# Performance work log

Measured on AMD Instinct MI355X. Metric: run time of the kernel, lower is better.

The kernel has to match this reference:

```python
import jax, jax.numpy as jnp
import numpy as np

N = 100000
E = 3200000
IN_C, HID_C, OUT_C = 128, 128, 64


def setup_inputs() -> dict:
    key = jax.random.key(0)
    k_x, k_e, k_w1, k_w2 = jax.random.split(key, 4)
    x = jax.random.normal(k_x, (N, IN_C), dtype=jnp.float32)
    edge_index = jax.random.randint(k_e, (2, E), 0, N, dtype=jnp.int64)
    # GCNConv uses Glorot-init weight [in, out] and zero bias
    W1 = jax.random.normal(k_w1, (IN_C, HID_C), dtype=jnp.float32) * (1.0 / np.sqrt(IN_C))
    b1 = jnp.zeros((HID_C,), dtype=jnp.float32)
    W2 = jax.random.normal(k_w2, (HID_C, OUT_C), dtype=jnp.float32) * (1.0 / np.sqrt(HID_C))
    b2 = jnp.zeros((OUT_C,), dtype=jnp.float32)
    return {"x": x, "edge_index": edge_index, "W1": W1, "b1": b1, "W2": W2, "b2": b2}


def _gcn_norm(edge_index, n_nodes):
    """Add self-loops and compute symmetric normalization coefficients."""
    loop = jnp.arange(n_nodes, dtype=edge_index.dtype)
    src = jnp.concatenate([edge_index[0], loop])  # [E+N]
    dst = jnp.concatenate([edge_index[1], loop])  # [E+N]
    ones = jnp.ones(src.shape[0], dtype=jnp.float32)
    deg = jax.ops.segment_sum(ones, dst, num_segments=n_nodes)  # in-degree w/ self loops
    dinv = jnp.where(deg > 0, jax.lax.rsqrt(deg), 0.0)
    norm = dinv[src] * dinv[dst]  # [E+N]
    return src, dst, norm


def _gcn_conv(x, W, b, src, dst, norm, n_nodes):
    h = x @ W                                   # [N, out] dense transform first (PyG order)
    msg = norm[:, None] * h[src]                # gather + scale  [E+N, out]
    out = jax.ops.segment_sum(msg, dst, num_segments=n_nodes)  # scatter-add
    return out + b


def reference(x, edge_index, W1, b1, W2, b2):
    src, dst, norm = _gcn_norm(edge_index, N)
    h = _gcn_conv(x, W1, b1, src, dst, norm, N)
    h = jax.nn.relu(h)
    out = _gcn_conv(h, W2, b2, src, dst, norm, N)
    return out
```

## Files before the change

### kernel.cpp

```cpp
#include <hip/hip_runtime.h>

typedef unsigned int u32;
typedef unsigned short u16;
typedef unsigned long long u64;
typedef __bf16 bf16x8 __attribute__((ext_vector_type(8)));
typedef float floatx4 __attribute__((ext_vector_type(4)));
typedef float floatx2 __attribute__((ext_vector_type(2)));
typedef u32 u32x2 __attribute__((ext_vector_type(2)));
typedef u32 u32x4 __attribute__((ext_vector_type(4)));


__device__ __forceinline__ u16 f2bf(float f) {
  u32 u = __float_as_uint(f);
  u += 0x7fffu + ((u >> 16) & 1u);
  return (u16)(u >> 16);
}
__device__ __forceinline__ float bflo(u32 v) { return __uint_as_float(v << 16); }
__device__ __forceinline__ float bfhi(u32 v) { return __uint_as_float(v & 0xffff0000u); }
__device__ __forceinline__ floatx2 bf2(u32 v) {
  floatx2 r; r.x = bflo(v); r.y = bfhi(v); return r;
}

#define SLICE_SH 10
#define SL (1 << SLICE_SH)
#define MAXNS 128
#define NBBIN 320
#define BTH 512
#define SRC_BITS 17

__device__ __forceinline__ void gemm1_body(const float* __restrict__ X,
                                           const float* __restrict__ W,
                                           u16* __restrict__ Y, int nrows,
                                           int bid, u16* Wt) {
  constexpr int K = 128, OUT = 128, NT = 8, LDW = 136;
  int tid = threadIdx.x;
  for (int idx = tid; idx < K * OUT; idx += BTH) {
    int k = idx >> 7, n = idx & 127;
    Wt[n * LDW + k] = f2bf(W[idx]);
  }
  __syncthreads();
  int lane = tid & 63, wave = tid >> 6;
  int quad = lane >> 4, low = lane & 15;
  int mBase = bid * 128 + wave * 16;
  int m = mBase + low;
  int ml = (m < nrows) ? m : (nrows - 1);
  floatx4 acc[NT];
#pragma unroll
  for (int i = 0; i < NT; i++) acc[i] = (floatx4)0.0f;
#pragma unroll
  for (int kb = 0; kb < 4; kb++) {
    int k0 = kb * 32 + quad * 8;
    floatx4 p0 = *(const floatx4*)(X + (size_t)ml * K + k0);
    floatx4 p1 = *(const floatx4*)(X + (size_t)ml * K + k0 + 4);
    union { bf16x8 v; u16 s[8]; } au;
#pragma unroll
    for (int j = 0; j < 4; j++) { au.s[j] = f2bf(p0[j]); au.s[4 + j] = f2bf(p1[j]); }
#pragma unroll
    for (int nt = 0; nt < NT; nt++) {
      bf16x8 b = *(const bf16x8*)(&Wt[(nt * 16 + low) * LDW + k0]);
      acc[nt] = __builtin_amdgcn_mfma_f32_16x16x32_bf16(au.v, b, acc[nt], 0, 0, 0);
    }
  }
#pragma unroll
  for (int nt = 0; nt < NT; nt++) {
    int col = nt * 16 + low;
#pragma unroll
    for (int r = 0; r < 4; r++) {
      int row = mBase + quad * 4 + r;
      if (row < nrows) Y[(size_t)row * OUT + col] = f2bf(acc[nt][r]);
    }
  }
}

__device__ __forceinline__ void bin_body(const int* __restrict__ ei,
                                         int* __restrict__ scur,
                                         u32* __restrict__ stA, u32* __restrict__ stB,
                                         int splitS, int cap, int e, int ns,
                                         int bid, int* hist, int* curs) {
  int per = (e + NBBIN - 1) / NBBIN;
  int e0 = bid * per;
  int e1 = e0 + per; if (e1 > e) e1 = e;
  for (int t = threadIdx.x; t < ns; t += BTH) hist[t] = 0;
  __syncthreads();
  for (int i = e0 + threadIdx.x; i < e1; i += BTH) {
    int d = ei[e + i];
    atomicAdd(&hist[d >> SLICE_SH], 1);
  }
  __syncthreads();
  for (int t = threadIdx.x; t < ns; t += BTH)
    curs[t] = atomicAdd(&scur[t], hist[t]);
  __syncthreads();
  int i = e0 + threadIdx.x;
  for (; i + 3 * BTH < e1; i += 4 * BTH) {
    int d[4], s[4], pos[4];
#pragma unroll
    for (int p = 0; p < 4; p++) {
      int ii = i + BTH * p;
      s[p] = ei[ii]; d[p] = ei[e + ii];
    }
#pragma unroll
    for (int p = 0; p < 4; p++) pos[p] = atomicAdd(&curs[d[p] >> SLICE_SH], 1);
#pragma unroll
    for (int p = 0; p < 4; p++) {
      int sl = d[p] >> SLICE_SH;
      u32* st = (sl < splitS) ? stA + (size_t)sl * cap : stB + (size_t)(sl - splitS) * cap;
      st[pos[p]] = ((u32)(d[p] & (SL - 1)) << SRC_BITS) | (u32)s[p];
    }
  }
  for (; i < e1; i += BTH) {
    int s = ei[i], d = ei[e + i];
    int sl = d >> SLICE_SH;
    u32* st = (sl < splitS) ? stA + (size_t)sl * cap : stB + (size_t)(sl - splitS) * cap;
    st[atomicAdd(&curs[sl], 1)] = ((u32)(d & (SL - 1)) << SRC_BITS) | (u32)s;
  }
}

__global__ __launch_bounds__(BTH) void gemm1_bin(const float* __restrict__ X,
                                                 const float* __restrict__ W1,
                                                 u16* __restrict__ Y, int nrows, int nbGemm,
                                                 const int* __restrict__ ei,
                                                 int* __restrict__ scur,
                                                 u32* __restrict__ stA, u32* __restrict__ stB,
                                                 int splitS, int cap, int e, int ns) {
  __shared__ __attribute__((aligned(16))) char smbuf[128 * 136 * 2];
  int id = blockIdx.x;
  int small = (NBBIN < nbGemm) ? NBBIN : nbGemm;
  int isBin, bid;
  if (id < 2 * small) { isBin = !(id & 1); bid = id >> 1; }
  else { bid = small + (id - 2 * small); isBin = (NBBIN > nbGemm); }
  if (isBin) {
    int* hist = (int*)smbuf;
    int* curs = hist + MAXNS;
    bin_body(ei, scur, stA, stB, splitS, cap, e, ns, bid, hist, curs);
  } else {
    gemm1_body(X, W1, Y, nrows, bid, (u16*)smbuf);
  }
}

__global__ __launch_bounds__(1024) void fill_slice3(const u32* __restrict__ stA,
                                                    const u32* __restrict__ stB,
                                                    const int* __restrict__ scur,
                                                    int* __restrict__ rp,
                                                    float* __restrict__ dinv,
                                                    int* __restrict__ csr,
                                                    int splitS, int cap, int n, int ns) {
  __shared__ int cnt[SL];
  __shared__ int part[SL];
  __shared__ int sb[MAXNS];
  const int s = blockIdx.x;
  const int base = s << SLICE_SH;
  const int tid = threadIdx.x;
  cnt[tid] = 0;
  if (tid < MAXNS) sb[tid] = (tid < ns) ? scur[tid] : 0;
  __syncthreads();
  for (int off = 1; off < MAXNS; off <<= 1) {
    int v = 0;
    if (tid < MAXNS && tid >= off) v = sb[tid - off];
    __syncthreads();
    if (tid < MAXNS) sb[tid] += v;
    __syncthreads();
  }
  const int csrLo = s ? sb[s - 1] : 0;
  const int m = sb[s] - csrLo;
  if (s == ns - 1 && tid == 0) rp[n] = sb[ns - 1];
  const u32* st = (s < splitS) ? stA + (size_t)s * cap : stB + (size_t)(s - splitS) * cap;
  {
    int i = tid;
    for (; i + 7168 < m; i += 8192) {
      int b[8];
#pragma unroll
      for (int p = 0; p < 8; p++) b[p] = (int)(st[i + 1024 * p] >> SRC_BITS);
#pragma unroll
      for (int p = 0; p < 8; p++) atomicAdd(&cnt[b[p]], 1);
    }
    for (; i < m; i += 1024)
      atomicAdd(&cnt[(int)(st[i] >> SRC_BITS)], 1);
  }
  __syncthreads();
  int c0 = cnt[tid];
  part[tid] = c0;
  __syncthreads();
  for (int off = 1; off < SL; off <<= 1) {
    int t = (tid >= off) ? part[tid - off] : 0;
    __syncthreads();
    part[tid] += t;
    __syncthreads();
  }
  int p0 = csrLo + (tid ? part[tid - 1] : 0);
  __syncthreads();
  cnt[tid] = p0;
  int d0 = base + tid;
  if (d0 < n) { rp[d0] = p0; dinv[d0] = rsqrtf((float)(c0 + 1)); }
  __syncthreads();
  {
    int i = tid;
    for (; i + 7168 < m; i += 8192) {
      u32 pr[8]; int pos[8];
#pragma unroll
      for (int p = 0; p < 8; p++) pr[p] = st[i + 1024 * p];
#pragma unroll
      for (int p = 0; p < 8; p++)
        pos[p] = atomicAdd(&cnt[pr[p] >> SRC_BITS], 1);
#pragma unroll
      for (int p = 0; p < 8; p++) csr[pos[p]] = (int)(pr[p] & ((1u << SRC_BITS) - 1u));
    }
    for (; i < m; i += 1024) {
      u32 pr = st[i];
      int pos = atomicAdd(&cnt[pr >> SRC_BITS], 1);
      csr[pos] = (int)(pr & ((1u << SRC_BITS) - 1u));
    }
  }
}

__global__ __launch_bounds__(256) void agg128_g2(const u32* __restrict__ H,
                                                 const int* __restrict__ rp,
                                                 const int* __restrict__ cs,
                                                 const float* __restrict__ dinv,
                                                 const float* __restrict__ b1,
                                                 const float* __restrict__ W2,
                                                 u16* __restrict__ h2, int n) {
  __shared__ u16 Wt[64 * 136];
  __shared__ u16 Arow[16 * 136];
  const int tid = threadIdx.x;
  for (int idx = tid; idx < 128 * 64; idx += 256) {
    int k = idx >> 6, nn = idx & 63;
    Wt[nn * 136 + k] = f2bf(W2[idx]);
  }
  const int nodeBase = blockIdx.x * 4;
  const int wave = tid >> 6, lane = tid & 63;
  int node = nodeBase + wave;
  int nodeC = (node < n) ? node : (n - 1);
  int e4 = lane >> 4, c = lane & 15;
  int s0 = rp[nodeC], s1 = rp[nodeC + 1];
  floatx2 a2[4];
#pragma unroll
  for (int k = 0; k < 4; k++) a2[k] = (floatx2)0.0f;
  for (int base = s0; base < s1; base += 64) {
    int nb = s1 - base; if (nb > 64) nb = 64;
    int src = 0; float dv = 0.f;
    if (lane < nb) { src = cs[base + lane]; dv = dinv[src]; }
    for (int j = 0; j < nb; j += 16) {
      u32x4 v[4]; float w[4];
#pragma unroll
      for (int p = 0; p < 4; p++) {
        int idx = j + 4 * p + e4;
        int sj = __shfl(src, idx);
        w[p] = __shfl(dv, idx);
        v[p] = *(const u32x4*)(H + (size_t)sj * 64 + 4 * c);
      }
#pragma unroll
      for (int p = 0; p < 4; p++) {
        floatx2 wp; wp.x = w[p]; wp.y = w[p];
#pragma unroll
        for (int k = 0; k < 4; k++) {
          a2[k] += wp * bf2(v[p][k]);
        }
      }
    }
  }
#pragma unroll
  for (int k = 0; k < 4; k++) {
    a2[k].x += __shfl_xor(a2[k].x, 16);
    a2[k].y += __shfl_xor(a2[k].y, 16);
    a2[k].x += __shfl_xor(a2[k].x, 32);
    a2[k].y += __shfl_xor(a2[k].y, 32);
  }
  float ds = dinv[nodeC];
  u32x4 vs = *(const u32x4*)(H + (size_t)nodeC * 64 + 4 * c);
  floatx4 bb0 = *(const floatx4*)(b1 + 8 * c);
  floatx4 bb1 = *(const floatx4*)(b1 + 8 * c + 4);
  float r[8];
#pragma unroll
  for (int k = 0; k < 4; k++) {
    r[2 * k]     = ds * (a2[k].x + ds * bflo(vs[k]));
    r[2 * k + 1] = ds * (a2[k].y + ds * bfhi(vs[k]));
  }
#pragma unroll
  for (int k = 0; k < 4; k++) { r[k] += bb0[k]; r[4 + k] += bb1[k]; }
#pragma unroll
  for (int k = 0; k < 8; k++) r[k] = fmaxf(r[k], 0.f);
  if (e4 == 0) {
    union { u16 s[8]; u32x4 v; } pk;
#pragma unroll
    for (int k = 0; k < 8; k++) pk.s[k] = f2bf(r[k]);
    *(u32x4*)&Arow[wave * 136 + 8 * c] = pk.v;
  }
  __syncthreads();
  const int quad = e4, low = c;
  floatx4 acc = (floatx4)0.0f;
#pragma unroll
  for (int kb = 0; kb < 4; kb++) {
    int k0 = kb * 32 + quad * 8;
    bf16x8 af = *(const bf16x8*)&Arow[low * 136 + k0];
    bf16x8 bf = *(const bf16x8*)&Wt[(wave * 16 + low) * 136 + k0];
    acc = __builtin_amdgcn_mfma_f32_16x16x32_bf16(af, bf, acc, 0, 0, 0);
  }
  if (quad == 0) {
#pragma unroll
    for (int rI = 0; rI < 4; rI++) {
      int row = nodeBase + rI;
      if (row < n) h2[(size_t)row * 64 + wave * 16 + low] = f2bf(acc[rI]);
    }
  }
}

__global__ __launch_bounds__(256) void agg_64(const u16* __restrict__ Hu,
                                              const int* __restrict__ rp,
                                              const int* __restrict__ cs,
                                              const float* __restrict__ dinv,
                                              const float* __restrict__ b2,
                                              float* __restrict__ out, int n) {
  const u32* H = (const u32*)Hu;
  int node = blockIdx.x * 4 + (threadIdx.x >> 6);
  if (node >= n) return;
  int lane = threadIdx.x & 63;
  int e4 = lane >> 4, c = lane & 15;
  int s0 = rp[node], s1 = rp[node + 1];
  floatx2 a2[2];
  a2[0] = (floatx2)0.0f; a2[1] = (floatx2)0.0f;
  for (int base = s0; base < s1; base += 64) {
    int nb = s1 - base; if (nb > 64) nb = 64;
    int src = 0; float dv = 0.f;
    if (lane < nb) { src = cs[base + lane]; dv = dinv[src]; }
    for (int j = 0; j < nb; j += 16) {
      u32x2 v[4]; float w[4];
#pragma unroll
      for (int p = 0; p < 4; p++) {
        int idx = j + 4 * p + e4;
        int sj = __shfl(src, idx);
        w[p] = __shfl(dv, idx);
        v[p] = *(const u32x2*)(H + (size_t)sj * 32 + 2 * c);
      }
#pragma unroll
      for (int p = 0; p < 4; p++) {
        floatx2 wp; wp.x = w[p]; wp.y = w[p];
        a2[0] += wp * bf2(v[p].x);
        a2[1] += wp * bf2(v[p].y);
      }
    }
  }
#pragma unroll
  for (int k = 0; k < 2; k++) {
    a2[k].x += __shfl_xor(a2[k].x, 16);
    a2[k].y += __shfl_xor(a2[k].y, 16);
    a2[k].x += __shfl_xor(a2[k].x, 32);
    a2[k].y += __shfl_xor(a2[k].y, 32);
  }
  float ds = dinv[node];
  u32x2 vs = *(const u32x2*)(H + (size_t)node * 32 + 2 * c);
  floatx4 bf = *(const floatx4*)(b2 + 4 * c);
  if (e4 == 0) {
    floatx4 o;
    o[0] = ds * (a2[0].x + ds * bflo(vs.x)) + bf[0];
    o[1] = ds * (a2[0].y + ds * bfhi(vs.x)) + bf[1];
    o[2] = ds * (a2[1].x + ds * bflo(vs.y)) + bf[2];
    o[3] = ds * (a2[1].y + ds * bfhi(vs.y)) + bf[3];
    *(floatx4*)(out + (size_t)node * 64 + 4 * c) = o;
  }
}


extern "C" void kernel_launch(void* const* d_in, const int* in_sizes, int n_in,
                              void* d_out, int out_size, void* d_ws, size_t ws_size,
                              hipStream_t stream) {
  const float* x  = (const float*)d_in[0];
  const int*   ei = (const int*)d_in[1];
  const float* W1 = (const float*)d_in[2];
  const float* b1 = (const float*)d_in[3];
  const float* W2 = (const float*)d_in[4];
  const float* b2 = (const float*)d_in[5];
  const int N = in_sizes[0] / 128;
  const int E = in_sizes[1] / 2;
  const int NS = (N + SL - 1) >> SLICE_SH;

  int CAP = (E + NS - 1) / NS;
  CAP += CAP / 8;
  size_t doutSlots = (size_t)out_size / 4;
  int SPLIT = (int)(doutSlots / (size_t)CAP);
  if (SPLIT > NS) SPLIT = NS;

  auto al = [](size_t v) { return (v + 255) & ~(size_t)255; };
  char* ws = (char*)d_ws;
  size_t o = 0;
  int*   scur  = (int*)(ws + o);  o += 512;
  int*   rp    = (int*)(ws + o);  o += al((size_t)(N + 1) * 4);
  float* dinv  = (float*)(ws + o); o += al((size_t)N * 4);
  int*   csr   = (int*)(ws + o);  o += al((size_t)E * 4);
  u16*   h     = (u16*)(ws + o);  o += al((size_t)N * 128 * 2);
  u16*   h2    = (u16*)(ws + o);  o += al((size_t)N * 128 * 2);
  u32* stA = (u32*)d_out;
  u32* stB = (u32*)h2;

  const int nbGemm = (N + 127) / 128;

  hipMemsetAsync(scur, 0, 512, stream);
  gemm1_bin<<<NBBIN + nbGemm, BTH, 0, stream>>>(x, W1, h, N, nbGemm,
                                                ei, scur, stA, stB, SPLIT, CAP, E, NS);
  fill_slice3<<<NS, 1024, 0, stream>>>(stA, stB, scur, rp, dinv, csr, SPLIT, CAP, N, NS);
  agg128_g2<<<(N + 3) / 4, 256, 0, stream>>>((const u32*)h, rp, csr, dinv, b1, W2, h2, N);
  agg_64<<<(N + 3) / 4, 256, 0, stream>>>(h2, rp, csr, dinv, b2, (float*)d_out, N);
}
```

Before: 368.8 us.

## Halve CSR slice size and stage slice edges in LDS for counting sort

Node slices shrink from 1024 to 512 nodes, so there are twice as many slices and the edges of each slice (about 16k) fit in shared memory. The fill kernel copies the slice's packed edges into LDS once, then runs both the histogram pass and the scatter pass from LDS instead of reading global memory twice. The binning kernel gets half as many bin blocks. The risks are that the shared staging array (about 120KB) limits occupancy to one block per CU, and there is no check that a slice's edge count fits in CAPMAX.

```diff
diff --git a/kernel.cpp b/kernel.cpp
--- a/kernel.cpp
+++ b/kernel.cpp
@@ -21,12 +21,13 @@
   floatx2 r; r.x = bflo(v); r.y = bfhi(v); return r;
 }
 
-#define SLICE_SH 10
+#define SLICE_SH 9
 #define SL (1 << SLICE_SH)
-#define MAXNS 128
-#define NBBIN 320
+#define MAXNS 256
+#define NBBIN 160
 #define BTH 512
 #define SRC_BITS 17
+#define CAPMAX 30000
 
 __device__ __forceinline__ void gemm1_body(const float* __restrict__ X,
                                            const float* __restrict__ W,
@@ -137,20 +138,21 @@
   }
 }
 
-__global__ __launch_bounds__(1024) void fill_slice3(const u32* __restrict__ stA,
+__global__ __launch_bounds__(1024) void fill_slice5(const u32* __restrict__ stA,
                                                     const u32* __restrict__ stB,
                                                     const int* __restrict__ scur,
                                                     int* __restrict__ rp,
                                                     float* __restrict__ dinv,
                                                     int* __restrict__ csr,
                                                     int splitS, int cap, int n, int ns) {
+  __shared__ u32 stg[CAPMAX];
   __shared__ int cnt[SL];
   __shared__ int part[SL];
   __shared__ int sb[MAXNS];
   const int s = blockIdx.x;
   const int base = s << SLICE_SH;
   const int tid = threadIdx.x;
-  cnt[tid] = 0;
+  if (tid < SL) cnt[tid] = 0;
   if (tid < MAXNS) sb[tid] = (tid < ns) ? scur[tid] : 0;
   __syncthreads();
   for (int off = 1; off < MAXNS; off <<= 1) {
@@ -164,51 +166,31 @@
   const int m = sb[s] - csrLo;
   if (s == ns - 1 && tid == 0) rp[n] = sb[ns - 1];
   const u32* st = (s < splitS) ? stA + (size_t)s * cap : stB + (size_t)(s - splitS) * cap;
-  {
-    int i = tid;
-    for (; i + 7168 < m; i += 8192) {
-      int b[8];
-#pragma unroll
-      for (int p = 0; p < 8; p++) b[p] = (int)(st[i + 1024 * p] >> SRC_BITS);
-#pragma unroll
-      for (int p = 0; p < 8; p++) atomicAdd(&cnt[b[p]], 1);
-    }
-    for (; i < m; i += 1024)
-      atomicAdd(&cnt[(int)(st[i] >> SRC_BITS)], 1);
-  }
-  __syncthreads();
-  int c0 = cnt[tid];
-  part[tid] = c0;
+  for (int i = tid; i < m; i += 1024) stg[i] = st[i];
+  __syncthreads();
+  for (int i = tid; i < m; i += 1024)
+    atomicAdd(&cnt[stg[i] >> SRC_BITS], 1);
+  __syncthreads();
+  int c0 = (tid < SL) ? cnt[tid] : 0;
+  if (tid < SL) part[tid] = c0;
   __syncthreads();
   for (int off = 1; off < SL; off <<= 1) {
-    int t = (tid >= off) ? part[tid - off] : 0;
+    int t = (tid < SL && tid >= off) ? part[tid - off] : 0;
     __syncthreads();
-    part[tid] += t;
+    if (tid < SL) part[tid] += t;
     __syncthreads();
   }
-  int p0 = csrLo + (tid ? part[tid - 1] : 0);
-  __syncthreads();
-  cnt[tid] = p0;
-  int d0 = base + tid;
-  if (d0 < n) { rp[d0] = p0; dinv[d0] = rsqrtf((float)(c0 + 1)); }
-  __syncthreads();
-  {
-    int i = tid;
-    for (; i + 7168 < m; i += 8192) {
-      u32 pr[8]; int pos[8];
-#pragma unroll
-      for (int p = 0; p < 8; p++) pr[p] = st[i + 1024 * p];
-#pragma unroll
-      for (int p = 0; p < 8; p++)
-        pos[p] = atomicAdd(&cnt[pr[p] >> SRC_BITS], 1);
-#pragma unroll
-      for (int p = 0; p < 8; p++) csr[pos[p]] = (int)(pr[p] & ((1u << SRC_BITS) - 1u));
-    }
-    for (; i < m; i += 1024) {
-      u32 pr = st[i];
-      int pos = atomicAdd(&cnt[pr >> SRC_BITS], 1);
-      csr[pos] = (int)(pr & ((1u << SRC_BITS) - 1u));
-    }
+  if (tid < SL) {
+    int p0 = csrLo + (tid ? part[tid - 1] : 0);
+    cnt[tid] = p0;
+    int d0 = base + tid;
+    if (d0 < n) { rp[d0] = p0; dinv[d0] = rsqrtf((float)(c0 + 1)); }
+  }
+  __syncthreads();
+  for (int i = tid; i < m; i += 1024) {
+    u32 pr = stg[i];
+    int pos = atomicAdd(&cnt[pr >> SRC_BITS], 1);
+    csr[pos] = (int)(pr & ((1u << SRC_BITS) - 1u));
   }
 }
 
@@ -382,7 +364,7 @@
   auto al = [](size_t v) { return (v + 255) & ~(size_t)255; };
   char* ws = (char*)d_ws;
   size_t o = 0;
-  int*   scur  = (int*)(ws + o);  o += 512;
+  int*   scur  = (int*)(ws + o);  o += 1024;
   int*   rp    = (int*)(ws + o);  o += al((size_t)(N + 1) * 4);
   float* dinv  = (float*)(ws + o); o += al((size_t)N * 4);
   int*   csr   = (int*)(ws + o);  o += al((size_t)E * 4);
@@ -393,10 +375,10 @@
 
   const int nbGemm = (N + 127) / 128;
 
-  hipMemsetAsync(scur, 0, 512, stream);
+  hipMemsetAsync(scur, 0, 1024, stream);
   gemm1_bin<<<NBBIN + nbGemm, BTH, 0, stream>>>(x, W1, h, N, nbGemm,
                                                 ei, scur, stA, stB, SPLIT, CAP, E, NS);
-  fill_slice3<<<NS, 1024, 0, stream>>>(stA, stB, scur, rp, dinv, csr, SPLIT, CAP, N, NS);
+  fill_slice5<<<NS, 1024, 0, stream>>>(stA, stB, scur, rp, dinv, csr, SPLIT, CAP, N, NS);
   agg128_g2<<<(N + 3) / 4, 256, 0, stream>>>((const u32*)h, rp, csr, dinv, b1, W2, h2, N);
   agg_64<<<(N + 3) / 4, 256, 0, stream>>>(h2, rp, csr, dinv, b2, (float*)d_out, N);
 }
```

After: 380.4 us. 3.1% more time.
